# Kernel optimization log

Measured on AMD Instinct MI355X. Metric: run time of the kernel, lower is better.

Reference implementation:

```python
import jax, jax.numpy as jnp
import numpy as np
from jax import lax

B, C, CI, H, W_SP = 8, 64, 3, 224, 224  # batch, per-channel groups, in-chans per group, spatial
K, STRIDE = 5, 2


def setup_inputs() -> dict:
    key = jax.random.key(0)
    kx, kw = jax.random.split(key)
    x = jax.random.normal(kx, (B, C, CI, H, W_SP), dtype=jnp.float32)
    # one Conv2d(3->1, k=5, stride=2, bias=False) per output channel -> stacked [C, CI, K, K]
    fan_in = CI * K * K
    bound = 1.0 / np.sqrt(fan_in)
    W = jax.random.uniform(kw, (C, CI, K, K), dtype=jnp.float32, minval=-bound, maxval=bound)
    return {"x": x, "W": W}


def reference(x, W):
    # x: [B, C, CI, H, W]; each of the C groups has its own 3->1 conv (weights W[c]).
    # Equivalent to a single grouped conv: input [B, C*CI, H, W], feature_group_count=C.
    b, c, ci, h, w = x.shape
    x2 = x.reshape(b, c * ci, h, w)
    out = lax.conv_general_dilated(
        x2, W,
        window_strides=(STRIDE, STRIDE),
        padding="VALID",
        feature_group_count=c,
        dimension_numbers=("NCHW", "OIHW", "NCHW"),
    )  # [B, C, H_out, W_out]
    return out
```

## Files before the change

kernel.cpp:

```cpp
#include <hip/hip_runtime.h>

#define BATCH 8
#define CH 64
#define CIN 3
#define HIN 224
#define WIN 224
#define KSZ 5
#define STRIDE 2
#define HO 110
#define WO 110
#define HW (HIN * WIN)

#define TPB 128
#define RING 12
#define HALF_OUT 55
#define NWG (BATCH * CH * 2)
#define LAST_IN 112
#define NW 75

typedef float float2a __attribute__((ext_vector_type(2)));

__device__ __forceinline__ void gload16(const float* src, float* ldsdst) {
    __builtin_amdgcn_global_load_lds(
        (const __attribute__((address_space(1))) void*)src,
        (__attribute__((address_space(3))) void*)ldsdst, 16, 0, 0);
}

__global__ __launch_bounds__(TPB) void conv5_ring_kernel(
    const float* __restrict__ x,
    const float* __restrict__ Wt,
    float* __restrict__ out)
{
    __shared__ float xs[CIN][RING][WIN];
    __shared__ float wsh[NW];

    const int wg  = blockIdx.x;
    const int swz = (wg & 7) * (NWG >> 3) + (wg >> 3);
    const int bc   = swz >> 1;
    const int half = swz & 1;
    const int c = bc & (CH - 1);
    const int tid = threadIdx.x;
    const int lane = tid & 63;
    const int wid  = tid >> 6;

    const float* gplane = x + (size_t)bc * (CIN * HW) + (size_t)(half * 110) * WIN;

    if (tid < NW) wsh[tid] = Wt[c * NW + tid];
    __syncthreads();
    float wr[NW];
#pragma unroll
    for (int i = 0; i < NW; ++i) wr[i] = wsh[i];

#pragma unroll
    for (int r = 0; r < 10; ++r) {
        if ((r & 1) == wid) {
#pragma unroll
            for (int ci = 0; ci < CIN; ++ci) {
                const float* src = gplane + (size_t)ci * HW + (size_t)r * WIN + lane * 4;
                if (lane < 56) gload16(src, &xs[ci][r][0]);
            }
        }
    }

    const int p = tid;
    float* orow = out + (size_t)bc * (HO * WO) + (size_t)(half * HALF_OUT) * WO + p;

    for (int j = 0; j < HALF_OUT; ++j) {
        {
            const int virt = 2 * j + 10 + wid;
            const int rsrc = virt > LAST_IN ? LAST_IN : virt;
            const int slot = virt % RING;
#pragma unroll
            for (int ci = 0; ci < CIN; ++ci) {
                const float* src = gplane + (size_t)ci * HW + (size_t)rsrc * WIN + lane * 4;
                if (lane < 56) gload16(src, &xs[ci][slot][0]);
            }
        }

        asm volatile("s_waitcnt vmcnt(9)" ::: "memory");
        __builtin_amdgcn_sched_barrier(0);
        __builtin_amdgcn_s_barrier();
        __builtin_amdgcn_sched_barrier(0);

        if (p < WO) {
            const int s0 = (2 * j) % RING;
            float a = 0.f;
#pragma unroll
            for (int ci = 0; ci < CIN; ++ci) {
#pragma unroll
                for (int kh = 0; kh < KSZ; ++kh) {
                    int sk = s0 + kh; if (sk >= RING) sk -= RING;
                    const float* rp = &xs[ci][sk][2 * p];
                    float2a v01 = *(const float2a*)rp;
                    float2a v23 = *(const float2a*)(rp + 2);
                    float   v4  = rp[4];
                    const float* w = wr + ci * 25 + kh * 5;
                    a = fmaf(v01.x, w[0], a);
                    a = fmaf(v01.y, w[1], a);
                    a = fmaf(v23.x, w[2], a);
                    a = fmaf(v23.y, w[3], a);
                    a = fmaf(v4,    w[4], a);
                }
            }
            orow[(size_t)j * WO] = a;
        }

        asm volatile("s_waitcnt lgkmcnt(0)" ::: "memory");
        __builtin_amdgcn_sched_barrier(0);
        __builtin_amdgcn_s_barrier();
        __builtin_amdgcn_sched_barrier(0);
    }

    asm volatile("s_waitcnt vmcnt(0)" ::: "memory");
}

extern "C" void kernel_launch(void* const* d_in, const int* in_sizes, int n_in,
                              void* d_out, int out_size, void* d_ws, size_t ws_size,
                              hipStream_t stream)
{
    const float* x  = (const float*)d_in[0];
    const float* Wt = (const float*)d_in[1];
    float* out = (float*)d_out;

    conv5_ring_kernel<<<dim3(NWG), dim3(TPB), 0, stream>>>(x, Wt, out);
}
```

Before: 70.83 us.

## Switch to single-wave workgroups with two outputs per lane and barrier-free ring

The workgroup shrinks from two waves to one, so each lane computes two adjacent output columns from float4 LDS reads, and the per-row s_barriers are removed. The ring buffer grows to 14 rows so two new input rows can be prefetched per iteration while the waits rely only on vmcnt and lgkmcnt counters. Weights are loaded straight from global memory into registers instead of being staged in LDS. Per-channel partial accumulators add ILP. The risks are higher LDS per wave, which may lower occupancy, and more vector register pressure.

```diff
diff --git a/kernel.cpp b/kernel.cpp
--- a/kernel.cpp
+++ b/kernel.cpp
@@ -11,13 +11,14 @@
 #define WO 110
 #define HW (HIN * WIN)
 
-#define TPB 128
-#define RING 12
+#define TPB 64
+#define RING 14
 #define HALF_OUT 55
 #define NWG (BATCH * CH * 2)
 #define LAST_IN 112
 #define NW 75
 
+typedef float float4a __attribute__((ext_vector_type(4)));
 typedef float float2a __attribute__((ext_vector_type(2)));
 
 __device__ __forceinline__ void gload16(const float* src, float* ldsdst) {
@@ -26,89 +27,87 @@
         (__attribute__((address_space(3))) void*)ldsdst, 16, 0, 0);
 }
 
-__global__ __launch_bounds__(TPB) void conv5_ring_kernel(
+__global__ __launch_bounds__(TPB) void conv5_wave_kernel(
     const float* __restrict__ x,
     const float* __restrict__ Wt,
     float* __restrict__ out)
 {
     __shared__ float xs[CIN][RING][WIN];
-    __shared__ float wsh[NW];
 
     const int wg  = blockIdx.x;
     const int swz = (wg & 7) * (NWG >> 3) + (wg >> 3);
     const int bc   = swz >> 1;
     const int half = swz & 1;
     const int c = bc & (CH - 1);
-    const int tid = threadIdx.x;
-    const int lane = tid & 63;
-    const int wid  = tid >> 6;
+    const int l = threadIdx.x;
 
     const float* gplane = x + (size_t)bc * (CIN * HW) + (size_t)(half * 110) * WIN;
 
-    if (tid < NW) wsh[tid] = Wt[c * NW + tid];
-    __syncthreads();
     float wr[NW];
 #pragma unroll
-    for (int i = 0; i < NW; ++i) wr[i] = wsh[i];
+    for (int i = 0; i < NW; ++i) wr[i] = Wt[c * NW + i];
 
 #pragma unroll
     for (int r = 0; r < 10; ++r) {
-        if ((r & 1) == wid) {
 #pragma unroll
-            for (int ci = 0; ci < CIN; ++ci) {
-                const float* src = gplane + (size_t)ci * HW + (size_t)r * WIN + lane * 4;
-                if (lane < 56) gload16(src, &xs[ci][r][0]);
-            }
+        for (int ci = 0; ci < CIN; ++ci) {
+            if (l < 56) gload16(gplane + (size_t)ci * HW + (size_t)r * WIN + 4 * l,
+                                &xs[ci][r][0]);
         }
     }
 
-    const int p = tid;
-    float* orow = out + (size_t)bc * (HO * WO) + (size_t)(half * HALF_OUT) * WO + p;
+    int s0 = 0, sA = 10, sB = 11;
+    float* orow = out + (size_t)bc * (HO * WO) + (size_t)(half * HALF_OUT) * WO + 2 * l;
 
     for (int j = 0; j < HALF_OUT; ++j) {
-        {
-            const int virt = 2 * j + 10 + wid;
-            const int rsrc = virt > LAST_IN ? LAST_IN : virt;
-            const int slot = virt % RING;
+        const int vA = 2 * j + 10, vB = 2 * j + 11;
+        const int rA = vA > LAST_IN ? LAST_IN : vA;
+        const int rB = vB > LAST_IN ? LAST_IN : vB;
+
+        asm volatile("s_waitcnt lgkmcnt(0)" ::: "memory");
+        __builtin_amdgcn_sched_barrier(0);
 #pragma unroll
-            for (int ci = 0; ci < CIN; ++ci) {
-                const float* src = gplane + (size_t)ci * HW + (size_t)rsrc * WIN + lane * 4;
-                if (lane < 56) gload16(src, &xs[ci][slot][0]);
+        for (int ci = 0; ci < CIN; ++ci) {
+            if (l < 56) {
+                gload16(gplane + (size_t)ci * HW + (size_t)rA * WIN + 4 * l, &xs[ci][sA][0]);
+                gload16(gplane + (size_t)ci * HW + (size_t)rB * WIN + 4 * l, &xs[ci][sB][0]);
             }
         }
-
-        asm volatile("s_waitcnt vmcnt(9)" ::: "memory");
-        __builtin_amdgcn_sched_barrier(0);
-        __builtin_amdgcn_s_barrier();
+        asm volatile("s_waitcnt vmcnt(20)" ::: "memory");
         __builtin_amdgcn_sched_barrier(0);
 
-        if (p < WO) {
-            const int s0 = (2 * j) % RING;
-            float a = 0.f;
+        if (l < 55) {
+            float a0[CIN], a1[CIN];
+#pragma unroll
+            for (int ci = 0; ci < CIN; ++ci) { a0[ci] = 0.f; a1[ci] = 0.f; }
 #pragma unroll
             for (int ci = 0; ci < CIN; ++ci) {
 #pragma unroll
                 for (int kh = 0; kh < KSZ; ++kh) {
                     int sk = s0 + kh; if (sk >= RING) sk -= RING;
-                    const float* rp = &xs[ci][sk][2 * p];
-                    float2a v01 = *(const float2a*)rp;
-                    float2a v23 = *(const float2a*)(rp + 2);
-                    float   v4  = rp[4];
+                    const float* rp = &xs[ci][sk][4 * l];
+                    float4a v0 = *(const float4a*)rp;
+                    float4a v1 = *(const float4a*)(rp + 4);
                     const float* w = wr + ci * 25 + kh * 5;
-                    a = fmaf(v01.x, w[0], a);
-                    a = fmaf(v01.y, w[1], a);
-                    a = fmaf(v23.x, w[2], a);
-                    a = fmaf(v23.y, w[3], a);
-                    a = fmaf(v4,    w[4], a);
+                    a0[ci] = fmaf(v0.x, w[0], a0[ci]);
+                    a0[ci] = fmaf(v0.y, w[1], a0[ci]);
+                    a0[ci] = fmaf(v0.z, w[2], a0[ci]);
+                    a0[ci] = fmaf(v0.w, w[3], a0[ci]);
+                    a0[ci] = fmaf(v1.x, w[4], a0[ci]);
+                    a1[ci] = fmaf(v0.z, w[0], a1[ci]);
+                    a1[ci] = fmaf(v0.w, w[1], a1[ci]);
+                    a1[ci] = fmaf(v1.x, w[2], a1[ci]);
+                    a1[ci] = fmaf(v1.y, w[3], a1[ci]);
+                    a1[ci] = fmaf(v1.z, w[4], a1[ci]);
                 }
             }
-            orow[(size_t)j * WO] = a;
+            float2a st = {(a0[0] + a0[1]) + a0[2], (a1[0] + a1[1]) + a1[2]};
+            *(float2a*)(orow + (size_t)j * WO) = st;
         }
 
-        asm volatile("s_waitcnt lgkmcnt(0)" ::: "memory");
-        __builtin_amdgcn_sched_barrier(0);
-        __builtin_amdgcn_s_barrier();
-        __builtin_amdgcn_sched_barrier(0);
+        s0 += 2; if (s0 >= RING) s0 -= RING;
+        sA += 2; if (sA >= RING) sA -= RING;
+        sB += 2; if (sB >= RING) sB -= RING;
     }
 
     asm volatile("s_waitcnt vmcnt(0)" ::: "memory");
@@ -122,5 +121,5 @@
     const float* Wt = (const float*)d_in[1];
     float* out = (float*)d_out;
 
-    conv5_ring_kernel<<<dim3(NWG), dim3(TPB), 0, stream>>>(x, Wt, out);
+    conv5_wave_kernel<<<dim3(NWG), dim3(TPB), 0, stream>>>(x, Wt, out);
 }
```

New measurement: 72.65 us. 1.03x slower.
